# Kernel tuning notes

Hardware: AMD Instinct MI355X
Metric: run time of the kernel (lower is better)

The kernel has to match this reference:

```python
import jax, jax.numpy as jnp
import numpy as np

B = 8192          # batch of scenes
H = 20            # human_num
O = 10            # other_robot_num
IN = 13           # input_dim
SELF = 6          # self_state_dim
AG = IN - SELF    # agent_state_dim = 7
E1, E2 = 256, 128 # wr_dims / wh_dims
HID = 32          # hardcoded hidden_channels in Graphgnn
FIN = 128         # final_state_dim
P1, P2, P3 = 256, 128, 1  # planning_dims
NE = 8            # number of hetero edge types
# edge-type index convention:
# 0 robot->human, 1 human->robot, 2 other->robot, 3 robot->other,
# 4 other->human, 5 human->other, 6 human->human, 7 other->other


def setup_inputs() -> dict:
    key = jax.random.key(0)
    ks = iter(jax.random.split(key, 40))
    def nrm(shape, scale=0.05):
        return jax.random.normal(next(ks), shape, jnp.float32) * scale
    inp = {}
    inp["state"] = jax.random.normal(next(ks), (B, H + O, IN), jnp.float32)
    inp["dropout"] = 0  # unused by forward (kept for signature fidelity)
    # w_r: SELF -> E1 -> E2 (last_relu=True)
    inp["wr_W0"] = nrm((SELF, E1)); inp["wr_b0"] = nrm((E1,))
    inp["wr_W1"] = nrm((E1, E2));   inp["wr_b1"] = nrm((E2,))
    # w_h: AG -> E1 -> E2
    inp["wh_W0"] = nrm((AG, E1));   inp["wh_b0"] = nrm((E1,))
    inp["wh_W1"] = nrm((E1, E2));   inp["wh_b1"] = nrm((E2,))
    # w_o: AG -> E1 -> E2
    inp["wo_W0"] = nrm((AG, E1));   inp["wo_b0"] = nrm((E1,))
    inp["wo_W1"] = nrm((E1, E2));   inp["wo_b1"] = nrm((E2,))
    # per-edge-type GraphConv params (PyG GraphConv: lin_rel has bias, lin_root has none)
    inp["c1_relW"]  = nrm((NE, E2, HID)); inp["c1_relb"]  = nrm((NE, HID))
    inp["c1_rootW"] = nrm((NE, E2, HID))
    inp["c2_relW"]  = nrm((NE, HID, FIN)); inp["c2_relb"]  = nrm((NE, FIN))
    inp["c2_rootW"] = nrm((NE, HID, FIN))
    # value_net: FIN -> P1 -> P2 -> P3 (no final relu)
    inp["v_W0"] = nrm((FIN, P1)); inp["v_b0"] = nrm((P1,))
    inp["v_W1"] = nrm((P1, P2));  inp["v_b1"] = nrm((P2,))
    inp["v_W2"] = nrm((P2, P3));  inp["v_b2"] = nrm((P3,))
    return inp


def _mlp2(x, W0, b0, W1, b1, last_relu):
    h = jax.nn.relu(x @ W0 + b0)
    h = h @ W1 + b1
    return jax.nn.relu(h) if last_relu else h


def _hetero_conv(xr, xh, xo, relW, relb, rootW):
    # xr: [B,1,D], xh: [B,H,D], xo: [B,O,D]
    # GraphConv per edge type: out_dst = lin_root(x_dst) + lin_rel(sum of src messages)
    # graph is complete bipartite (sence) / complete-minus-self (affect),
    # so aggregations are closed-form sums.
    lin  = lambda x, i: jnp.einsum('bnd,do->bno', x, relW[i]) + relb[i]
    root = lambda x, i: jnp.einsum('bnd,do->bno', x, rootW[i])
    sh = xh.sum(axis=1, keepdims=True)  # [B,1,D] sum over humans
    so = xo.sum(axis=1, keepdims=True)  # [B,1,D] sum over other robots
    # robot receives: human->robot (1), other->robot (2)
    out_r = lin(sh, 1) + root(xr, 1) + lin(so, 2) + root(xr, 2)
    # human receives: robot->human (0), other->human (4), human->human (6)
    out_h = (lin(xr, 0) + root(xh, 0)
             + lin(so, 4) + root(xh, 4)
             + lin(sh - xh, 6) + root(xh, 6))
    # other receives: robot->other (3), human->other (5), other->other (7)
    out_o = (lin(xr, 3) + root(xo, 3)
             + lin(sh, 5) + root(xo, 5)
             + lin(so - xo, 7) + root(xo, 7))
    return out_r, out_h, out_o


def reference(state, dropout,
              wr_W0, wr_b0, wr_W1, wr_b1,
              wh_W0, wh_b0, wh_W1, wh_b1,
              wo_W0, wo_b0, wo_W1, wo_b1,
              c1_relW, c1_relb, c1_rootW,
              c2_relW, c2_relb, c2_rootW,
              v_W0, v_b0, v_W1, v_b1, v_W2, v_b2):
    self_state = state[:, 0, :SELF]          # [B, SELF]
    human_states = state[:, :H, SELF:]       # [B, H, AG]
    other_states = state[:, H:, SELF:]       # [B, O, AG]
    er = _mlp2(self_state, wr_W0, wr_b0, wr_W1, wr_b1, True)[:, None, :]  # [B,1,E2]
    eh = _mlp2(human_states, wh_W0, wh_b0, wh_W1, wh_b1, True)            # [B,H,E2]
    eo = _mlp2(other_states, wo_W0, wo_b0, wo_W1, wo_b1, True)            # [B,O,E2]
    r, h, o = _hetero_conv(er, eh, eo, c1_relW, c1_relb, c1_rootW)
    r, h, o = jax.nn.relu(r), jax.nn.relu(h), jax.nn.relu(o)
    r, h, o = _hetero_conv(r, h, o, c2_relW, c2_relb, c2_rootW)
    r = jax.nn.relu(r)
    hr = r[:, 0, :]                           # robot node per scene, [B, FIN]
    v = jax.nn.relu(hr @ v_W0 + v_b0)
    v = jax.nn.relu(v @ v_W1 + v_b1)
    v = v @ v_W2 + v_b2                       # [B, 1]
    return v
```

## Files before the change

### kernel.cpp

```cpp
#include <hip/hip_runtime.h>
#include <hip/hip_bf16.h>
#include <stdint.h>

#define BATCH 8192
#define NSTATE 30
#define DIN 13
#define E1 256
#define E2 128

typedef short bf16x8 __attribute__((ext_vector_type(8)));
typedef float f32x4 __attribute__((ext_vector_type(4)));
typedef __bf16 bf16x2_t __attribute__((ext_vector_type(2)));

__device__ __forceinline__ unsigned short f2b(float f) {
    return __builtin_bit_cast(unsigned short, (__bf16)f);
}
__device__ __forceinline__ float b2f(unsigned short b) {
    return __uint_as_float((unsigned)b << 16);
}
__device__ __forceinline__ unsigned pack2(float a, float b) {
    bf16x2_t v = {(__bf16)fmaxf(a, 0.f), (__bf16)fmaxf(b, 0.f)};
    return __builtin_bit_cast(unsigned, v);
}
__device__ __forceinline__ unsigned pack2n(float a, float b) {
    bf16x2_t v = {(__bf16)a, (__bf16)b};
    return __builtin_bit_cast(unsigned, v);
}

__device__ __forceinline__ f32x4 pin_f4(f32x4 v) {
    uint4 u = __builtin_bit_cast(uint4, v);
    asm volatile("" : "+v"(u.x), "+v"(u.y), "+v"(u.z), "+v"(u.w));
    return __builtin_bit_cast(f32x4, u);
}

__device__ __forceinline__ float wcat_val(int k, int m, const float* relW, const float* rootW) {
    int part = k >> 7, c = k & 127, grp = m >> 5, mm = m & 31;
    int off = c * 32 + mm;
    if (part == 0) return (grp == 0) ? rootW[4096 + off] + rootW[8192 + off]
                        : (grp == 1) ? relW[off] : relW[3*4096 + off];
    if (part == 1) return (grp == 0) ? relW[1*4096 + off]
                        : (grp == 1) ? relW[6*4096 + off] : relW[5*4096 + off];
    return (grp == 0) ? relW[2*4096 + off]
         : (grp == 1) ? relW[4*4096 + off] : relW[7*4096 + off];
}
__device__ __forceinline__ float wc2_val(int k, int n, const float* relW, const float* rootW) {
    int grp = k >> 5, kk = k & 31;
    int off = kk * 128 + n;
    if (grp == 0) return rootW[4096 + off] + rootW[8192 + off];
    if (grp == 1) return relW[4096 + off];
    return relW[8192 + off];
}

__global__ void k_prep(const float* __restrict__ c1_relW, const float* __restrict__ c1_relb,
                       const float* __restrict__ c1_rootW,
                       const float* __restrict__ c2_relW, const float* __restrict__ c2_relb,
                       const float* __restrict__ c2_rootW,
                       const float* __restrict__ wh_W0, const float* __restrict__ wh_W1,
                       const float* __restrict__ wo_W0, const float* __restrict__ wo_W1,
                       const float* __restrict__ wr_W0, const float* __restrict__ wr_W1,
                       const float* __restrict__ v_W0, const float* __restrict__ v_W1,
                       const float* __restrict__ b0h, const float* __restrict__ b0o,
                       const float* __restrict__ b0r,
                       float* __restrict__ bcat, float* __restrict__ bc2,
                       unsigned short* __restrict__ W0b_h, unsigned short* __restrict__ W0b_o,
                       unsigned short* __restrict__ W0b_r,
                       unsigned short* __restrict__ W1f_h, unsigned short* __restrict__ W1f_o,
                       unsigned short* __restrict__ W1f_r,
                       unsigned short* __restrict__ Mf_h, unsigned short* __restrict__ Mf_o,
                       unsigned short* __restrict__ Wcatf, unsigned short* __restrict__ Wc2f,
                       unsigned short* __restrict__ vW0f, unsigned short* __restrict__ vW1f)
{
    int gid = blockIdx.x * blockDim.x + threadIdx.x;
    int gsz = gridDim.x * blockDim.x;

    for (int i = gid; i < 96; i += gsz) {
        int grp = i >> 5, mm = i & 31;
        float v;
        if (grp == 0)      v = c1_relb[32 + mm] + c1_relb[64 + mm];
        else if (grp == 1) v = c1_relb[mm] + c1_relb[128 + mm] + c1_relb[192 + mm];
        else               v = c1_relb[96 + mm] + c1_relb[160 + mm] + c1_relb[224 + mm];
        bcat[i] = v;
    }
    for (int i = gid; i < 128; i += gsz) bc2[i] = c2_relb[128 + i] + c2_relb[256 + i];

    for (int i = gid; i < 2048; i += gsz) {
        int n = i >> 3, j = i & 7;
        W0b_h[i] = (j < 7) ? f2b(wh_W0[j * 256 + n]) : f2b(b0h[n]);
        W0b_o[i] = (j < 7) ? f2b(wo_W0[j * 256 + n]) : f2b(b0o[n]);
        W0b_r[i] = (j < 6) ? f2b(wr_W0[j * 256 + n])
                 : (j == 6) ? f2b(b0r[n]) : (unsigned short)0;
    }
    for (int i = gid; i < 32768; i += gsz) {
        int j = i & 7, l = (i >> 3) & 63, nt = (i >> 9) & 7, ks = i >> 12;
        int kk = ((j >> 2) * 8 + ks) * 16 + (l >> 4) * 4 + (j & 3);
        int n = nt * 16 + (l & 15);
        W1f_h[i] = f2b(wh_W1[kk * 128 + n]);
        W1f_o[i] = f2b(wo_W1[kk * 128 + n]);
        W1f_r[i] = f2b(wr_W1[kk * 128 + n]);
    }
    for (int i = gid; i < 4096; i += gsz) {
        int j = i & 7, l = (i >> 3) & 63, nt = (i >> 9) & 1, ks = i >> 10;
        int kk = ((j >> 2) * 4 + ks) * 16 + (l >> 4) * 4 + (j & 3);
        int n = nt * 16 + (l & 15);
        int i0 = kk * 32 + n;
        Mf_h[i] = f2b(c1_rootW[i0] + c1_rootW[4*4096 + i0] + c1_rootW[6*4096 + i0] - c1_relW[6*4096 + i0]);
        Mf_o[i] = f2b(c1_rootW[3*4096 + i0] + c1_rootW[5*4096 + i0] + c1_rootW[7*4096 + i0] - c1_relW[7*4096 + i0]);
    }
    for (int i = gid; i < 36864; i += gsz) {
        int j = i & 7, l = (i >> 3) & 63, rem = i >> 9;
        int nt = rem % 6, ks = rem / 6;
        int k = ks * 32 + (l >> 4) * 8 + j;
        int n = nt * 16 + (l & 15);
        Wcatf[i] = f2b(wcat_val(k, n, c1_relW, c1_rootW));
    }
    for (int i = gid; i < 12288; i += gsz) {
        int j = i & 7, l = (i >> 3) & 63, rem = i >> 9;
        int nt = rem & 7, ks = rem >> 3;
        int k = ks * 32 + (l >> 4) * 8 + j;
        int n = nt * 16 + (l & 15);
        Wc2f[i] = f2b(wc2_val(k, n, c2_relW, c2_rootW));
    }
    for (int i = gid; i < 32768; i += gsz) {
        int j = i & 7, l = (i >> 3) & 63, rem = i >> 9;
        int nt = rem & 15, ks = rem >> 4;
        int k = ks * 32 + (l >> 4) * 8 + j;
        int n = nt * 16 + (l & 15);
        vW0f[i] = f2b(v_W0[k * 256 + n]);
    }
    for (int i = gid; i < 32768; i += gsz) {
        int j = i & 7, l = (i >> 3) & 63, rem = i >> 9;
        int nt = rem & 7, ks = rem >> 3;
        int k = ks * 32 + (l >> 4) * 8 + j;
        int n = nt * 16 + (l & 15);
        vW1f[i] = f2b(v_W1[k * 128 + n]);
    }
}

#define SM_W0   0
#define SM_MF   4096
#define SM_W1   12288
#define SM_B1   77824
#define SM_HS   78336
#define SM_SZ   (78336 + 16 * 16 * 136 * 2)

template<int NPB, int NODE0, int INOFF, int INDIM, bool TAIL>
__device__ __forceinline__ void mlp_blockE(
    int blkrow0, const float* __restrict__ state,
    const unsigned short* __restrict__ W0b_g,
    const unsigned short* __restrict__ W1f_g, const float* __restrict__ b1,
    const unsigned short* __restrict__ Mf_g,
    unsigned short* __restrict__ tR, float* __restrict__ sumB,
    unsigned short* __restrict__ eR, char* smem)
{
    unsigned short* W0s = (unsigned short*)(smem + SM_W0);
    unsigned short* Mfs = (unsigned short*)(smem + SM_MF);
    unsigned short* W1s = (unsigned short*)(smem + SM_W1);
    float* b1s          = (float*)(smem + SM_B1);

    const int t = threadIdx.x;
    const int lane = t & 63;
    const int w = t >> 6;
    const int l15 = lane & 15;
    const int quad = lane >> 4;
    const int R0 = blkrow0 + w * 64;
    unsigned short* ew = (unsigned short*)(smem + SM_HS) + w * (16 * 136);

    if (t < 256) ((uint4*)W0s)[t] = ((const uint4*)W0b_g)[t];
    if (t >= 256 && t < 384) b1s[t - 256] = b1[t - 256];
    #pragma unroll
    for (int i = 0; i < 4; ++i)
        ((uint4*)W1s)[t + 1024 * i] = ((const uint4*)W1f_g)[t + 1024 * i];
    if constexpr (TAIL) {
        if (t >= 512 && t < 1024) ((uint4*)Mfs)[t - 512] = ((const uint4*)Mf_g)[t - 512];
    }
    __syncthreads();

    f32x4 bias1[8];
    #pragma unroll
    for (int nt = 0; nt < 8; ++nt) {
        float4 bb = *(const float4*)(b1s + nt * 16 + quad * 4);
        bias1[nt] = pin_f4((f32x4){bb.x, bb.y, bb.z, bb.w});
    }

    float s0 = 0.f, s1 = 0.f;
    int bcur = R0 / NPB;

    float xf[INDIM];
    #pragma unroll 1
    for (int dummy = 0; dummy < 1; ++dummy) {
        if (quad == 0) {
            int grow = R0 + l15;
            int b = grow / NPB;
            int n = grow - b * NPB + NODE0;
            const float* xp = state + ((size_t)b * NSTATE + n) * DIN + INOFF;
            #pragma unroll
            for (int j = 0; j < INDIM; ++j) xf[j] = xp[j];
        }
    }

    for (int sub = 0; sub < 4; ++sub) {
        const int wrow0 = R0 + sub * 16;

        bf16x8 bx = {};
        if (quad == 0) {
            #pragma unroll
            for (int j = 0; j < INDIM; ++j)
                bx[j] = (short)f2b(xf[j]);
            bx[INDIM] = (short)0x3F80;
        }
        if (sub < 3 && quad == 0) {
            int grow = wrow0 + 16 + l15;
            int b = grow / NPB;
            int n = grow - b * NPB + NODE0;
            const float* xp = state + ((size_t)b * NSTATE + n) * DIN + INOFF;
            #pragma unroll
            for (int j = 0; j < INDIM; ++j) xf[j] = xp[j];
        }

        f32x4 a1[16];
        #pragma unroll
        for (int nt = 0; nt < 16; ++nt) {
            bf16x8 aw = {};
            if (quad == 0)
                aw = *(const bf16x8*)(W0s + (nt * 16 + l15) * 8);
            f32x4 c = {0.f, 0.f, 0.f, 0.f};
            a1[nt] = __builtin_amdgcn_mfma_f32_16x16x32_bf16(aw, bx, c, 0, 0, 0);
        }

        bf16x8 bh[8];
        #pragma unroll
        for (int ks = 0; ks < 8; ++ks) {
            uint4 u;
            u.x = pack2(a1[ks][0], a1[ks][1]);
            u.y = pack2(a1[ks][2], a1[ks][3]);
            u.z = pack2(a1[ks + 8][0], a1[ks + 8][1]);
            u.w = pack2(a1[ks + 8][2], a1[ks + 8][3]);
            bh[ks] = __builtin_bit_cast(bf16x8, u);
        }

        f32x4 acc[8];
        #pragma unroll
        for (int nt = 0; nt < 8; ++nt) acc[nt] = bias1[nt];
        #pragma unroll
        for (int ks = 0; ks < 8; ++ks) {
            #pragma unroll
            for (int nt = 0; nt < 8; ++nt) {
                bf16x8 aw = *(const bf16x8*)(W1s + ((ks * 8 + nt) * 64 + lane) * 8);
                acc[nt] = __builtin_amdgcn_mfma_f32_16x16x32_bf16(aw, bh[ks], acc[nt], 0, 0, 0);
            }
        }

        uint2 pv[8];
        #pragma unroll
        for (int nt = 0; nt < 8; ++nt)
            pv[nt] = (uint2){pack2(acc[nt][0], acc[nt][1]), pack2(acc[nt][2], acc[nt][3])};

        if constexpr (TAIL) {
            __asm__ __volatile__("s_waitcnt lgkmcnt(0)" ::: "memory");
            #pragma unroll
            for (int nt = 0; nt < 8; ++nt)
                *(uint2*)(ew + l15 * 136 + nt * 16 + quad * 4) = pv[nt];

            f32x4 tacc[2] = {{0.f,0.f,0.f,0.f},{0.f,0.f,0.f,0.f}};
            #pragma unroll
            for (int ks = 0; ks < 4; ++ks) {
                uint4 ua;
                ua.x = pv[ks].x; ua.y = pv[ks].y;
                ua.z = pv[ks + 4].x; ua.w = pv[ks + 4].y;
                bf16x8 ae = __builtin_bit_cast(bf16x8, ua);
                #pragma unroll
                for (int nt = 0; nt < 2; ++nt) {
                    bf16x8 bm = *(const bf16x8*)(Mfs + ((ks * 2 + nt) * 64 + lane) * 8);
                    tacc[nt] = __builtin_amdgcn_mfma_f32_16x16x32_bf16(bm, ae, tacc[nt], 0, 0, 0);
                }
            }
            #pragma unroll
            for (int nt = 0; nt < 2; ++nt) {
                uint2 tv = {pack2n(tacc[nt][0], tacc[nt][1]), pack2n(tacc[nt][2], tacc[nt][3])};
                *(uint2*)(tR + (size_t)(wrow0 + l15) * 32 + nt * 16 + quad * 4) = tv;
            }

            #pragma unroll
            for (int r = 0; r < 16; ++r) {
                int b = (wrow0 + r) / NPB;
                if (b != bcur) {
                    bool interior = (bcur * NPB >= R0) && ((bcur + 1) * NPB <= R0 + 64);
                    float* dst = sumB + (size_t)bcur * 128 + 2 * lane;
                    if (interior) { dst[0] = s0; dst[1] = s1; }
                    else { atomicAdd(dst, s0); atomicAdd(dst + 1, s1); }
                    s0 = 0.f; s1 = 0.f; bcur = b;
                }
                unsigned v = *(const unsigned*)(ew + r * 136 + lane * 2);
                s0 += b2f((unsigned short)v);
                s1 += b2f((unsigned short)(v >> 16));
            }
            if (sub == 3) {
                bool interior = (bcur * NPB >= R0) && ((bcur + 1) * NPB <= R0 + 64);
                float* dst = sumB + (size_t)bcur * 128 + 2 * lane;
                if (interior) { dst[0] = s0; dst[1] = s1; }
                else { atomicAdd(dst, s0); atomicAdd(dst + 1, s1); }
            }
        } else {
            #pragma unroll
            for (int nt = 0; nt < 8; ++nt)
                *(uint2*)(eR + (size_t)(wrow0 + l15) * 128 + nt * 16 + quad * 4) = pv[nt];
        }
        __asm__ __volatile__("" ::: "memory");
    }
}

__global__ __launch_bounds__(1024, 1) void k_mlpE(
    const float* __restrict__ state,
    const unsigned short* __restrict__ W0b_h,
    const unsigned short* __restrict__ W1f_h, const float* __restrict__ b1_h,
    const unsigned short* __restrict__ Mf_h, unsigned short* __restrict__ tR_h,
    float* __restrict__ shB,
    const unsigned short* __restrict__ W0b_o,
    const unsigned short* __restrict__ W1f_o, const float* __restrict__ b1_o,
    const unsigned short* __restrict__ Mf_o, unsigned short* __restrict__ tR_o,
    float* __restrict__ soB,
    const unsigned short* __restrict__ W0b_r,
    const unsigned short* __restrict__ W1f_r, const float* __restrict__ b1_r,
    unsigned short* __restrict__ eR)
{
    __shared__ __align__(16) char smem[SM_SZ];
    int bid = blockIdx.x;
    if (bid < 160)
        mlp_blockE<20, 0, 6, 7, true>(bid * 1024, state, W0b_h, W1f_h, b1_h,
                                      Mf_h, tR_h, shB, nullptr, smem);
    else if (bid < 240)
        mlp_blockE<10, 20, 6, 7, true>((bid - 160) * 1024, state, W0b_o, W1f_o, b1_o,
                                       Mf_o, tR_o, soB, nullptr, smem);
    else
        mlp_blockE<1, 0, 0, 6, false>((bid - 240) * 1024, state, W0b_r, W1f_r, b1_r,
                                      nullptr, nullptr, nullptr, eR, smem);
}

__global__ __launch_bounds__(256, 2) void k_tail(
    const unsigned short* __restrict__ eR,
    const float* __restrict__ shB, const float* __restrict__ soB,
    const unsigned short* __restrict__ tR_h, const unsigned short* __restrict__ tR_o,
    const unsigned short* __restrict__ Wcatf, const float* __restrict__ bcat,
    const unsigned short* __restrict__ Wc2f, const float* __restrict__ bc2,
    const unsigned short* __restrict__ vW0f, const float* __restrict__ vb0,
    const unsigned short* __restrict__ vW1f, const float* __restrict__ vb1,
    const float* __restrict__ vW2, const float* __restrict__ vb2,
    float* __restrict__ out)
{
    __shared__ __align__(16) char sm[33024];
    unsigned short* Ub  = (unsigned short*)(sm);
    unsigned short* V1b = (unsigned short*)(sm);
    unsigned short* Vb  = (unsigned short*)(sm + 12800);
    float* chL          = (float*)(sm + 16128);
    float* coL          = (float*)(sm + 18176);
    unsigned short* Hb  = (unsigned short*)(sm + 20224);
    float* V2b          = (float*)(sm + 24576);

    const int t = threadIdx.x, lane = t & 63, w = t >> 6;
    const int l15 = lane & 15, quad = lane >> 4;
    const int b0 = blockIdx.x * 16;
    const int rowb = quad * 4;

    {
        int b = t >> 4, q = t & 15;
        ((uint4*)(Ub + b * 400))[q] = ((const uint4*)(eR + (size_t)(b0 + b) * 128))[q];
    }
    for (int idx = t; idx < 4096; idx += 256) {
        int b = idx >> 8, kk = idx & 255;
        float v = (kk < 128) ? shB[(size_t)(b0 + b) * 128 + kk]
                             : soB[(size_t)(b0 + b) * 128 + kk - 128];
        Ub[b * 400 + 128 + kk] = f2b(v);
    }
    __syncthreads();

    for (int nt = w; nt < 6; nt += 4) {
        float bias = bcat[nt * 16 + l15];
        f32x4 acc = {bias, bias, bias, bias};
        #pragma unroll
        for (int ks = 0; ks < 12; ++ks) {
            bf16x8 a = *(const bf16x8*)(Ub + l15 * 400 + ks * 32 + quad * 8);
            bf16x8 bw = *(const bf16x8*)(Wcatf + ((ks * 6 + nt) * 64 + lane) * 8);
            acc = __builtin_amdgcn_mfma_f32_16x16x32_bf16(a, bw, acc, 0, 0, 0);
        }
        int n = nt * 16 + l15;
        #pragma unroll
        for (int reg = 0; reg < 4; ++reg) {
            float v = acc[reg];
            int b = rowb + reg;
            if (n < 32)      Vb[b * 104 + n] = f2b(fmaxf(v, 0.f));
            else if (n < 64) chL[b * 32 + (n - 32)] = v;
            else             coL[b * 32 + (n - 64)] = v;
        }
    }
    __syncthreads();

    for (int idx = t; idx < 512; idx += 256) {
        int b = idx >> 5, m = idx & 31;
        float ch = chL[b * 32 + m];
        const unsigned short* p = tR_h + (size_t)(b0 + b) * 20 * 32 + m;
        float s = 0.f;
        #pragma unroll
        for (int n = 0; n < 20; ++n) s += fmaxf(ch + b2f(p[n * 32]), 0.f);
        Vb[b * 104 + 32 + m] = f2b(s);
        float co = coL[b * 32 + m];
        const unsigned short* p2 = tR_o + (size_t)(b0 + b) * 10 * 32 + m;
        float s2 = 0.f;
        #pragma unroll
        for (int n = 0; n < 10; ++n) s2 += fmaxf(co + b2f(p2[n * 32]), 0.f);
        Vb[b * 104 + 64 + m] = f2b(s2);
    }
    __syncthreads();

    {
        f32x4 acc[2];
        #pragma unroll
        for (int q = 0; q < 2; ++q) {
            int nt = w + q * 4;
            float bias = bc2[nt * 16 + l15];
            acc[q] = (f32x4){bias, bias, bias, bias};
        }
        #pragma unroll
        for (int ks = 0; ks < 3; ++ks) {
            bf16x8 a = *(const bf16x8*)(Vb + l15 * 104 + ks * 32 + quad * 8);
            #pragma unroll
            for (int q = 0; q < 2; ++q) {
                int nt = w + q * 4;
                bf16x8 bw = *(const bf16x8*)(Wc2f + ((ks * 8 + nt) * 64 + lane) * 8);
                acc[q] = __builtin_amdgcn_mfma_f32_16x16x32_bf16(a, bw, acc[q], 0, 0, 0);
            }
        }
        #pragma unroll
        for (int q = 0; q < 2; ++q) {
            int nt = w + q * 4;
            #pragma unroll
            for (int reg = 0; reg < 4; ++reg)
                Hb[(rowb + reg) * 136 + nt * 16 + l15] = f2b(fmaxf(acc[q][reg], 0.f));
        }
    }
    __syncthreads();

    {
        f32x4 acc[4];
        #pragma unroll
        for (int q = 0; q < 4; ++q) {
            int nt = w + q * 4;
            float bias = vb0[nt * 16 + l15];
            acc[q] = (f32x4){bias, bias, bias, bias};
        }
        #pragma unroll
        for (int ks = 0; ks < 4; ++ks) {
            bf16x8 a = *(const bf16x8*)(Hb + l15 * 136 + ks * 32 + quad * 8);
            #pragma unroll
            for (int q = 0; q < 4; ++q) {
                int nt = w + q * 4;
                bf16x8 bw = *(const bf16x8*)(vW0f + ((ks * 16 + nt) * 64 + lane) * 8);
                acc[q] = __builtin_amdgcn_mfma_f32_16x16x32_bf16(a, bw, acc[q], 0, 0, 0);
            }
        }
        __syncthreads();
        #pragma unroll
        for (int q = 0; q < 4; ++q) {
            int nt = w + q * 4;
            #pragma unroll
            for (int reg = 0; reg < 4; ++reg)
                V1b[(rowb + reg) * 264 + nt * 16 + l15] = f2b(fmaxf(acc[q][reg], 0.f));
        }
    }
    __syncthreads();

    {
        f32x4 acc[2];
        #pragma unroll
        for (int q = 0; q < 2; ++q) {
            int nt = w + q * 4;
            float bias = vb1[nt * 16 + l15];
            acc[q] = (f32x4){bias, bias, bias, bias};
        }
        #pragma unroll
        for (int ks = 0; ks < 8; ++ks) {
            bf16x8 a = *(const bf16x8*)(V1b + l15 * 264 + ks * 32 + quad * 8);
            #pragma unroll
            for (int q = 0; q < 2; ++q) {
                int nt = w + q * 4;
                bf16x8 bw = *(const bf16x8*)(vW1f + ((ks * 8 + nt) * 64 + lane) * 8);
                acc[q] = __builtin_amdgcn_mfma_f32_16x16x32_bf16(a, bw, acc[q], 0, 0, 0);
            }
        }
        #pragma unroll
        for (int q = 0; q < 2; ++q) {
            int nt = w + q * 4;
            #pragma unroll
            for (int reg = 0; reg < 4; ++reg)
                V2b[(rowb + reg) * 132 + nt * 16 + l15] = fmaxf(acc[q][reg], 0.f);
        }
    }
    __syncthreads();

    if (t < 128) {
        int b = t >> 3, j = t & 7;
        float v = 0.f;
        #pragma unroll
        for (int k = 0; k < 16; ++k)
            v = fmaf(V2b[b * 132 + j * 16 + k], vW2[j * 16 + k], v);
        v += __shfl_down(v, 4, 8);
        v += __shfl_down(v, 2, 8);
        v += __shfl_down(v, 1, 8);
        if (j == 0) out[b0 + b] = v + vb2[0];
    }
}

extern "C" void kernel_launch(void* const* d_in, const int* in_sizes, int n_in,
                              void* d_out, int out_size, void* d_ws, size_t ws_size,
                              hipStream_t stream)
{
    const float* state   = (const float*)d_in[0];
    const float* wr_W0   = (const float*)d_in[2];
    const float* wr_b0   = (const float*)d_in[3];
    const float* wr_W1   = (const float*)d_in[4];
    const float* wr_b1   = (const float*)d_in[5];
    const float* wh_W0   = (const float*)d_in[6];
    const float* wh_b0   = (const float*)d_in[7];
    const float* wh_W1   = (const float*)d_in[8];
    const float* wh_b1   = (const float*)d_in[9];
    const float* wo_W0   = (const float*)d_in[10];
    const float* wo_b0   = (const float*)d_in[11];
    const float* wo_W1   = (const float*)d_in[12];
    const float* wo_b1   = (const float*)d_in[13];
    const float* c1_relW = (const float*)d_in[14];
    const float* c1_relb = (const float*)d_in[15];
    const float* c1_rootW= (const float*)d_in[16];
    const float* c2_relW = (const float*)d_in[17];
    const float* c2_relb = (const float*)d_in[18];
    const float* c2_rootW= (const float*)d_in[19];
    const float* v_W0    = (const float*)d_in[20];
    const float* v_b0    = (const float*)d_in[21];
    const float* v_W1    = (const float*)d_in[22];
    const float* v_b1    = (const float*)d_in[23];
    const float* v_W2    = (const float*)d_in[24];
    const float* v_b2    = (const float*)d_in[25];

    char* ws = (char*)d_ws;
    size_t off = 0;
    auto alloc = [&](size_t bytes) -> char* {
        char* p = ws + off;
        off = (off + bytes + 255) & ~(size_t)255;
        return p;
    };
    float* shB  = (float*)alloc((size_t)BATCH * 128 * 4);
    float* soB  = (float*)alloc((size_t)BATCH * 128 * 4);
    unsigned short* tR_h = (unsigned short*)alloc((size_t)163840 * 32 * 2);
    unsigned short* tR_o = (unsigned short*)alloc((size_t)81920 * 32 * 2);
    unsigned short* eR   = (unsigned short*)alloc((size_t)BATCH * 128 * 2);
    float* bcat = (float*)alloc(96 * 4);
    float* bc2  = (float*)alloc(128 * 4);
    unsigned short* W0b_h = (unsigned short*)alloc(2048 * 2);
    unsigned short* W0b_o = (unsigned short*)alloc(2048 * 2);
    unsigned short* W0b_r = (unsigned short*)alloc(2048 * 2);
    unsigned short* W1f_h = (unsigned short*)alloc(32768 * 2);
    unsigned short* W1f_o = (unsigned short*)alloc(32768 * 2);
    unsigned short* W1f_r = (unsigned short*)alloc(32768 * 2);
    unsigned short* Mf_h  = (unsigned short*)alloc(4096 * 2);
    unsigned short* Mf_o  = (unsigned short*)alloc(4096 * 2);
    unsigned short* Wcatf = (unsigned short*)alloc(36864 * 2);
    unsigned short* Wc2f  = (unsigned short*)alloc(12288 * 2);
    unsigned short* vW0f  = (unsigned short*)alloc(32768 * 2);
    unsigned short* vW1f  = (unsigned short*)alloc(32768 * 2);
    (void)ws_size; (void)in_sizes; (void)n_in; (void)out_size;

    hipMemsetAsync(shB, 0, (size_t)2 * BATCH * 128 * 4, stream);

    k_prep<<<256, 256, 0, stream>>>(c1_relW, c1_relb, c1_rootW, c2_relW, c2_relb, c2_rootW,
                                    wh_W0, wh_W1, wo_W0, wo_W1, wr_W0, wr_W1, v_W0, v_W1,
                                    wh_b0, wo_b0, wr_b0,
                                    bcat, bc2, W0b_h, W0b_o, W0b_r, W1f_h, W1f_o, W1f_r,
                                    Mf_h, Mf_o, Wcatf, Wc2f, vW0f, vW1f);

    k_mlpE<<<248, 1024, 0, stream>>>(state,
                                     W0b_h, W1f_h, wh_b1, Mf_h, tR_h, shB,
                                     W0b_o, W1f_o, wo_b1, Mf_o, tR_o, soB,
                                     W0b_r, W1f_r, wr_b1, eR);

    k_tail<<<512, 256, 0, stream>>>(eR, shB, soB, tR_h, tR_o,
                                    Wcatf, bcat, Wc2f, bc2, vW0f, v_b0, vW1f, v_b1,
                                    v_W2, v_b2, (float*)d_out);
}
```

Measured before the change: 157.5 us.

## Switch encoder MLP to 32x32x16 MFMA tiles with bias folded into GEMM

Rewrites the per-node encoder MLP in k_mlpE to use 32x32x16 bf16 MFMA instead of 16x16x32. Each wave now handles two 32-row subtiles instead of four 16-row subtiles, and the first-layer output is fed straight into the second layer per 32-column chunk. The second-layer bias is folded in as an extra K-step that multiplies by a ones vector, replacing the preloaded bias registers. k_prep re-lays out W0, W1 and M to match the new fragment layout. This targets the weight-load and instruction overhead of small MFMA tiles, but raises register pressure (f32x16 accumulators) and adds an extra MFMA step for the bias.

```diff
diff --git a/kernel.cpp b/kernel.cpp
--- a/kernel.cpp
+++ b/kernel.cpp
@@ -10,6 +10,7 @@
 
 typedef short bf16x8 __attribute__((ext_vector_type(8)));
 typedef float f32x4 __attribute__((ext_vector_type(4)));
+typedef float f32x16 __attribute__((ext_vector_type(16)));
 typedef __bf16 bf16x2_t __attribute__((ext_vector_type(2)));
 
 __device__ __forceinline__ unsigned short f2b(float f) {
@@ -25,12 +26,6 @@
 __device__ __forceinline__ unsigned pack2n(float a, float b) {
     bf16x2_t v = {(__bf16)a, (__bf16)b};
     return __builtin_bit_cast(unsigned, v);
-}
-
-__device__ __forceinline__ f32x4 pin_f4(f32x4 v) {
-    uint4 u = __builtin_bit_cast(uint4, v);
-    asm volatile("" : "+v"(u.x), "+v"(u.y), "+v"(u.z), "+v"(u.w));
-    return __builtin_bit_cast(f32x4, u);
 }
 
 __device__ __forceinline__ float wcat_val(int k, int m, const float* relW, const float* rootW) {
@@ -61,6 +56,8 @@
                        const float* __restrict__ v_W0, const float* __restrict__ v_W1,
                        const float* __restrict__ b0h, const float* __restrict__ b0o,
                        const float* __restrict__ b0r,
+                       const float* __restrict__ b1h, const float* __restrict__ b1o,
+                       const float* __restrict__ b1r,
                        float* __restrict__ bcat, float* __restrict__ bc2,
                        unsigned short* __restrict__ W0b_h, unsigned short* __restrict__ W0b_o,
                        unsigned short* __restrict__ W0b_r,
@@ -83,26 +80,44 @@
     }
     for (int i = gid; i < 128; i += gsz) bc2[i] = c2_relb[128 + i] + c2_relb[256 + i];
 
-    for (int i = gid; i < 2048; i += gsz) {
-        int n = i >> 3, j = i & 7;
-        W0b_h[i] = (j < 7) ? f2b(wh_W0[j * 256 + n]) : f2b(b0h[n]);
-        W0b_o[i] = (j < 7) ? f2b(wo_W0[j * 256 + n]) : f2b(b0o[n]);
-        W0b_r[i] = (j < 6) ? f2b(wr_W0[j * 256 + n])
-                 : (j == 6) ? f2b(b0r[n]) : (unsigned short)0;
-    }
-    for (int i = gid; i < 32768; i += gsz) {
-        int j = i & 7, l = (i >> 3) & 63, nt = (i >> 9) & 7, ks = i >> 12;
-        int kk = ((j >> 2) * 8 + ks) * 16 + (l >> 4) * 4 + (j & 3);
-        int n = nt * 16 + (l & 15);
-        W1f_h[i] = f2b(wh_W1[kk * 128 + n]);
-        W1f_o[i] = f2b(wo_W1[kk * 128 + n]);
-        W1f_r[i] = f2b(wr_W1[kk * 128 + n]);
-    }
     for (int i = gid; i < 4096; i += gsz) {
-        int j = i & 7, l = (i >> 3) & 63, nt = (i >> 9) & 1, ks = i >> 10;
-        int kk = ((j >> 2) * 4 + ks) * 16 + (l >> 4) * 4 + (j & 3);
-        int n = nt * 16 + (l & 15);
-        int i0 = kk * 32 + n;
+        int j = i & 7, l = (i >> 3) & 63, nh = i >> 9;
+        int col = nh * 32 + (l & 31);
+        unsigned short vh = 0, vo = 0, vr = 0;
+        if (l < 32) {
+            vh = (j < 7) ? f2b(wh_W0[j * 256 + col]) : f2b(b0h[col]);
+            vo = (j < 7) ? f2b(wo_W0[j * 256 + col]) : f2b(b0o[col]);
+            vr = (j < 6) ? f2b(wr_W0[j * 256 + col])
+               : (j == 6) ? f2b(b0r[col]) : (unsigned short)0;
+        }
+        W0b_h[i] = vh; W0b_o[i] = vo; W0b_r[i] = vr;
+    }
+    for (int i = gid; i < 34816; i += gsz) {
+        int j = i & 7, l = (i >> 3) & 63, rem = i >> 9;
+        int nt = rem & 3, ks = rem >> 2;
+        int ecol = nt * 32 + (l & 31);
+        int hh = l >> 5;
+        unsigned short vh, vo, vr;
+        if (ks < 16) {
+            int r = (ks & 1) * 8 + j;
+            int hcol = (ks >> 1) * 32 + (r & 3) + 8 * (r >> 2) + 4 * hh;
+            vh = f2b(wh_W1[hcol * 128 + ecol]);
+            vo = f2b(wo_W1[hcol * 128 + ecol]);
+            vr = f2b(wr_W1[hcol * 128 + ecol]);
+        } else {
+            bool on = (l < 32) && (j == 0);
+            vh = on ? f2b(b1h[ecol]) : (unsigned short)0;
+            vo = on ? f2b(b1o[ecol]) : (unsigned short)0;
+            vr = on ? f2b(b1r[ecol]) : (unsigned short)0;
+        }
+        W1f_h[i] = vh; W1f_o[i] = vo; W1f_r[i] = vr;
+    }
+    for (int i = gid; i < 4096; i += gsz) {
+        int j = i & 7, l = (i >> 3) & 63, kt = i >> 9;
+        int hh = l >> 5, s = kt & 1, r = s * 8 + j;
+        int ecol = (kt >> 1) * 32 + (r & 3) + 8 * (r >> 2) + 4 * hh;
+        int tcol = l & 31;
+        int i0 = ecol * 32 + tcol;
         Mf_h[i] = f2b(c1_rootW[i0] + c1_rootW[4*4096 + i0] + c1_rootW[6*4096 + i0] - c1_relW[6*4096 + i0]);
         Mf_o[i] = f2b(c1_rootW[3*4096 + i0] + c1_rootW[5*4096 + i0] + c1_rootW[7*4096 + i0] - c1_relW[7*4096 + i0]);
     }
@@ -137,17 +152,16 @@
 }
 
 #define SM_W0   0
-#define SM_MF   4096
-#define SM_W1   12288
-#define SM_B1   77824
-#define SM_HS   78336
-#define SM_SZ   (78336 + 16 * 16 * 136 * 2)
+#define SM_MF   8192
+#define SM_W1   16384
+#define SM_HS   86016
+#define SM_SZ   (86016 + 16 * 16 * 136 * 2)
 
 template<int NPB, int NODE0, int INOFF, int INDIM, bool TAIL>
 __device__ __forceinline__ void mlp_blockE(
     int blkrow0, const float* __restrict__ state,
     const unsigned short* __restrict__ W0b_g,
-    const unsigned short* __restrict__ W1f_g, const float* __restrict__ b1,
+    const unsigned short* __restrict__ W1f_g,
     const unsigned short* __restrict__ Mf_g,
     unsigned short* __restrict__ tR, float* __restrict__ sumB,
     unsigned short* __restrict__ eR, char* smem)
@@ -155,155 +169,160 @@
     unsigned short* W0s = (unsigned short*)(smem + SM_W0);
     unsigned short* Mfs = (unsigned short*)(smem + SM_MF);
     unsigned short* W1s = (unsigned short*)(smem + SM_W1);
-    float* b1s          = (float*)(smem + SM_B1);
 
     const int t = threadIdx.x;
     const int lane = t & 63;
     const int w = t >> 6;
-    const int l15 = lane & 15;
-    const int quad = lane >> 4;
+    const int l31 = lane & 31;
+    const int hi = lane >> 5;
     const int R0 = blkrow0 + w * 64;
     unsigned short* ew = (unsigned short*)(smem + SM_HS) + w * (16 * 136);
 
-    if (t < 256) ((uint4*)W0s)[t] = ((const uint4*)W0b_g)[t];
-    if (t >= 256 && t < 384) b1s[t - 256] = b1[t - 256];
+    if (t < 512) ((uint4*)W0s)[t] = ((const uint4*)W0b_g)[t];
+    if constexpr (TAIL) {
+        if (t >= 512) ((uint4*)Mfs)[t - 512] = ((const uint4*)Mf_g)[t - 512];
+    }
     #pragma unroll
     for (int i = 0; i < 4; ++i)
         ((uint4*)W1s)[t + 1024 * i] = ((const uint4*)W1f_g)[t + 1024 * i];
-    if constexpr (TAIL) {
-        if (t >= 512 && t < 1024) ((uint4*)Mfs)[t - 512] = ((const uint4*)Mf_g)[t - 512];
-    }
+    if (t < 256) ((uint4*)W1s)[4096 + t] = ((const uint4*)W1f_g)[4096 + t];
     __syncthreads();
 
-    f32x4 bias1[8];
-    #pragma unroll
-    for (int nt = 0; nt < 8; ++nt) {
-        float4 bb = *(const float4*)(b1s + nt * 16 + quad * 4);
-        bias1[nt] = pin_f4((f32x4){bb.x, bb.y, bb.z, bb.w});
-    }
+    bf16x8 bones = {};
+    if (lane < 32) bones[0] = (short)0x3F80;
 
     float s0 = 0.f, s1 = 0.f;
     int bcur = R0 / NPB;
 
     float xf[INDIM];
-    #pragma unroll 1
-    for (int dummy = 0; dummy < 1; ++dummy) {
-        if (quad == 0) {
-            int grow = R0 + l15;
+    if (lane < 32) {
+        int grow = R0 + l31;
+        int b = grow / NPB;
+        int n = grow - b * NPB + NODE0;
+        const float* xp = state + ((size_t)b * NSTATE + n) * DIN + INOFF;
+        #pragma unroll
+        for (int j = 0; j < INDIM; ++j) xf[j] = xp[j];
+    }
+
+    for (int sub = 0; sub < 2; ++sub) {
+        const int wrow0 = R0 + sub * 32;
+
+        bf16x8 bx = {};
+        if (lane < 32) {
+            #pragma unroll
+            for (int j = 0; j < INDIM; ++j) bx[j] = (short)f2b(xf[j]);
+            bx[INDIM] = (short)0x3F80;
+        }
+        if (sub < 1 && lane < 32) {
+            int grow = wrow0 + 32 + l31;
             int b = grow / NPB;
             int n = grow - b * NPB + NODE0;
             const float* xp = state + ((size_t)b * NSTATE + n) * DIN + INOFF;
             #pragma unroll
             for (int j = 0; j < INDIM; ++j) xf[j] = xp[j];
         }
-    }
-
-    for (int sub = 0; sub < 4; ++sub) {
-        const int wrow0 = R0 + sub * 16;
-
-        bf16x8 bx = {};
-        if (quad == 0) {
-            #pragma unroll
-            for (int j = 0; j < INDIM; ++j)
-                bx[j] = (short)f2b(xf[j]);
-            bx[INDIM] = (short)0x3F80;
-        }
-        if (sub < 3 && quad == 0) {
-            int grow = wrow0 + 16 + l15;
-            int b = grow / NPB;
-            int n = grow - b * NPB + NODE0;
-            const float* xp = state + ((size_t)b * NSTATE + n) * DIN + INOFF;
-            #pragma unroll
-            for (int j = 0; j < INDIM; ++j) xf[j] = xp[j];
-        }
-
-        f32x4 a1[16];
-        #pragma unroll
-        for (int nt = 0; nt < 16; ++nt) {
-            bf16x8 aw = {};
-            if (quad == 0)
-                aw = *(const bf16x8*)(W0s + (nt * 16 + l15) * 8);
-            f32x4 c = {0.f, 0.f, 0.f, 0.f};
-            a1[nt] = __builtin_amdgcn_mfma_f32_16x16x32_bf16(aw, bx, c, 0, 0, 0);
-        }
-
-        bf16x8 bh[8];
-        #pragma unroll
-        for (int ks = 0; ks < 8; ++ks) {
-            uint4 u;
-            u.x = pack2(a1[ks][0], a1[ks][1]);
-            u.y = pack2(a1[ks][2], a1[ks][3]);
-            u.z = pack2(a1[ks + 8][0], a1[ks + 8][1]);
-            u.w = pack2(a1[ks + 8][2], a1[ks + 8][3]);
-            bh[ks] = __builtin_bit_cast(bf16x8, u);
-        }
-
-        f32x4 acc[8];
-        #pragma unroll
-        for (int nt = 0; nt < 8; ++nt) acc[nt] = bias1[nt];
-        #pragma unroll
-        for (int ks = 0; ks < 8; ++ks) {
-            #pragma unroll
-            for (int nt = 0; nt < 8; ++nt) {
-                bf16x8 aw = *(const bf16x8*)(W1s + ((ks * 8 + nt) * 64 + lane) * 8);
-                acc[nt] = __builtin_amdgcn_mfma_f32_16x16x32_bf16(aw, bh[ks], acc[nt], 0, 0, 0);
-            }
-        }
-
-        uint2 pv[8];
-        #pragma unroll
-        for (int nt = 0; nt < 8; ++nt)
-            pv[nt] = (uint2){pack2(acc[nt][0], acc[nt][1]), pack2(acc[nt][2], acc[nt][3])};
+
+        f32x16 acc[4];
+        #pragma unroll
+        for (int nt = 0; nt < 4; ++nt) { f32x16 z = {}; acc[nt] = z; }
+        #pragma unroll
+        for (int nh = 0; nh < 8; ++nh) {
+            bf16x8 aw0 = *(const bf16x8*)(W0s + (nh * 64 + lane) * 8);
+            f32x16 z = {};
+            f32x16 a1 = __builtin_amdgcn_mfma_f32_32x32x16_bf16(aw0, bx, z, 0, 0, 0);
+            uint4 ua, ub;
+            ua.x = pack2(a1[0], a1[1]);   ua.y = pack2(a1[2], a1[3]);
+            ua.z = pack2(a1[4], a1[5]);   ua.w = pack2(a1[6], a1[7]);
+            ub.x = pack2(a1[8], a1[9]);   ub.y = pack2(a1[10], a1[11]);
+            ub.z = pack2(a1[12], a1[13]); ub.w = pack2(a1[14], a1[15]);
+            bf16x8 bhA = __builtin_bit_cast(bf16x8, ua);
+            bf16x8 bhB = __builtin_bit_cast(bf16x8, ub);
+            #pragma unroll
+            for (int nt = 0; nt < 4; ++nt) {
+                bf16x8 aw = *(const bf16x8*)(W1s + (((2 * nh) * 4 + nt) * 64 + lane) * 8);
+                acc[nt] = __builtin_amdgcn_mfma_f32_32x32x16_bf16(aw, bhA, acc[nt], 0, 0, 0);
+            }
+            #pragma unroll
+            for (int nt = 0; nt < 4; ++nt) {
+                bf16x8 aw = *(const bf16x8*)(W1s + (((2 * nh + 1) * 4 + nt) * 64 + lane) * 8);
+                acc[nt] = __builtin_amdgcn_mfma_f32_32x32x16_bf16(aw, bhB, acc[nt], 0, 0, 0);
+            }
+        }
+        #pragma unroll
+        for (int nt = 0; nt < 4; ++nt) {
+            bf16x8 aw = *(const bf16x8*)(W1s + ((64 + nt) * 64 + lane) * 8);
+            acc[nt] = __builtin_amdgcn_mfma_f32_32x32x16_bf16(aw, bones, acc[nt], 0, 0, 0);
+        }
+
+        unsigned pvu[4][8];
+        #pragma unroll
+        for (int nt = 0; nt < 4; ++nt)
+            #pragma unroll
+            for (int p = 0; p < 8; ++p)
+                pvu[nt][p] = pack2(acc[nt][2 * p], acc[nt][2 * p + 1]);
 
         if constexpr (TAIL) {
-            __asm__ __volatile__("s_waitcnt lgkmcnt(0)" ::: "memory");
-            #pragma unroll
-            for (int nt = 0; nt < 8; ++nt)
-                *(uint2*)(ew + l15 * 136 + nt * 16 + quad * 4) = pv[nt];
-
-            f32x4 tacc[2] = {{0.f,0.f,0.f,0.f},{0.f,0.f,0.f,0.f}};
-            #pragma unroll
-            for (int ks = 0; ks < 4; ++ks) {
-                uint4 ua;
-                ua.x = pv[ks].x; ua.y = pv[ks].y;
-                ua.z = pv[ks + 4].x; ua.w = pv[ks + 4].y;
+            f32x16 tacc = {};
+            #pragma unroll
+            for (int kt = 0; kt < 8; ++kt) {
+                const int nt = kt >> 1, s = kt & 1;
+                uint4 ua = {pvu[nt][4 * s], pvu[nt][4 * s + 1],
+                            pvu[nt][4 * s + 2], pvu[nt][4 * s + 3]};
                 bf16x8 ae = __builtin_bit_cast(bf16x8, ua);
+                bf16x8 bm = *(const bf16x8*)(Mfs + (kt * 64 + lane) * 8);
+                tacc = __builtin_amdgcn_mfma_f32_32x32x16_bf16(bm, ae, tacc, 0, 0, 0);
+            }
+            {
+                unsigned short* tRrow = tR + (size_t)(wrow0 + l31) * 32 + 4 * hi;
                 #pragma unroll
-                for (int nt = 0; nt < 2; ++nt) {
-                    bf16x8 bm = *(const bf16x8*)(Mfs + ((ks * 2 + nt) * 64 + lane) * 8);
-                    tacc[nt] = __builtin_amdgcn_mfma_f32_16x16x32_bf16(bm, ae, tacc[nt], 0, 0, 0);
+                for (int q = 0; q < 4; ++q) {
+                    uint2 tv = {pack2n(tacc[4 * q], tacc[4 * q + 1]),
+                                pack2n(tacc[4 * q + 2], tacc[4 * q + 3])};
+                    *(uint2*)(tRrow + 8 * q) = tv;
                 }
             }
             #pragma unroll
-            for (int nt = 0; nt < 2; ++nt) {
-                uint2 tv = {pack2n(tacc[nt][0], tacc[nt][1]), pack2n(tacc[nt][2], tacc[nt][3])};
-                *(uint2*)(tR + (size_t)(wrow0 + l15) * 32 + nt * 16 + quad * 4) = tv;
-            }
-
-            #pragma unroll
-            for (int r = 0; r < 16; ++r) {
-                int b = (wrow0 + r) / NPB;
-                if (b != bcur) {
-                    bool interior = (bcur * NPB >= R0) && ((bcur + 1) * NPB <= R0 + 64);
-                    float* dst = sumB + (size_t)bcur * 128 + 2 * lane;
-                    if (interior) { dst[0] = s0; dst[1] = s1; }
-                    else { atomicAdd(dst, s0); atomicAdd(dst + 1, s1); }
-                    s0 = 0.f; s1 = 0.f; bcur = b;
+            for (int half = 0; half < 2; ++half) {
+                __asm__ __volatile__("s_waitcnt lgkmcnt(0)" ::: "memory");
+                if ((l31 >> 4) == half) {
+                    unsigned short* er = ew + (l31 & 15) * 136 + 4 * hi;
+                    #pragma unroll
+                    for (int nt = 0; nt < 4; ++nt)
+                        #pragma unroll
+                        for (int q = 0; q < 4; ++q)
+                            *(uint2*)(er + nt * 32 + 8 * q) =
+                                (uint2){pvu[nt][2 * q], pvu[nt][2 * q + 1]};
                 }
-                unsigned v = *(const unsigned*)(ew + r * 136 + lane * 2);
-                s0 += b2f((unsigned short)v);
-                s1 += b2f((unsigned short)(v >> 16));
-            }
-            if (sub == 3) {
+                const int grow0 = wrow0 + half * 16;
+                #pragma unroll
+                for (int r = 0; r < 16; ++r) {
+                    int b = (grow0 + r) / NPB;
+                    if (b != bcur) {
+                        bool interior = (bcur * NPB >= R0) && ((bcur + 1) * NPB <= R0 + 64);
+                        float* dst = sumB + (size_t)bcur * 128 + 2 * lane;
+                        if (interior) { dst[0] = s0; dst[1] = s1; }
+                        else { atomicAdd(dst, s0); atomicAdd(dst + 1, s1); }
+                        s0 = 0.f; s1 = 0.f; bcur = b;
+                    }
+                    unsigned v = *(const unsigned*)(ew + r * 136 + lane * 2);
+                    s0 += b2f((unsigned short)v);
+                    s1 += b2f((unsigned short)(v >> 16));
+                }
+            }
+            if (sub == 1) {
                 bool interior = (bcur * NPB >= R0) && ((bcur + 1) * NPB <= R0 + 64);
                 float* dst = sumB + (size_t)bcur * 128 + 2 * lane;
                 if (interior) { dst[0] = s0; dst[1] = s1; }
                 else { atomicAdd(dst, s0); atomicAdd(dst + 1, s1); }
             }
         } else {
-            #pragma unroll
-            for (int nt = 0; nt < 8; ++nt)
-                *(uint2*)(eR + (size_t)(wrow0 + l15) * 128 + nt * 16 + quad * 4) = pv[nt];
+            unsigned short* eRrow = eR + (size_t)(wrow0 + l31) * 128 + 4 * hi;
+            #pragma unroll
+            for (int nt = 0; nt < 4; ++nt)
+                #pragma unroll
+                for (int q = 0; q < 4; ++q)
+                    *(uint2*)(eRrow + nt * 32 + 8 * q) =
+                        (uint2){pvu[nt][2 * q], pvu[nt][2 * q + 1]};
         }
         __asm__ __volatile__("" ::: "memory");
     }
@@ -312,27 +331,27 @@
 __global__ __launch_bounds__(1024, 1) void k_mlpE(
     const float* __restrict__ state,
     const unsigned short* __restrict__ W0b_h,
-    const unsigned short* __restrict__ W1f_h, const float* __restrict__ b1_h,
+    const unsigned short* __restrict__ W1f_h,
     const unsigned short* __restrict__ Mf_h, unsigned short* __restrict__ tR_h,
     float* __restrict__ shB,
     const unsigned short* __restrict__ W0b_o,
-    const unsigned short* __restrict__ W1f_o, const float* __restrict__ b1_o,
+    const unsigned short* __restrict__ W1f_o,
     const unsigned short* __restrict__ Mf_o, unsigned short* __restrict__ tR_o,
     float* __restrict__ soB,
     const unsigned short* __restrict__ W0b_r,
-    const unsigned short* __restrict__ W1f_r, const float* __restrict__ b1_r,
+    const unsigned short* __restrict__ W1f_r,
     unsigned short* __restrict__ eR)
 {
     __shared__ __align__(16) char smem[SM_SZ];
     int bid = blockIdx.x;
     if (bid < 160)
-        mlp_blockE<20, 0, 6, 7, true>(bid * 1024, state, W0b_h, W1f_h, b1_h,
+        mlp_blockE<20, 0, 6, 7, true>(bid * 1024, state, W0b_h, W1f_h,
                                       Mf_h, tR_h, shB, nullptr, smem);
     else if (bid < 240)
-        mlp_blockE<10, 20, 6, 7, true>((bid - 160) * 1024, state, W0b_o, W1f_o, b1_o,
+        mlp_blockE<10, 20, 6, 7, true>((bid - 160) * 1024, state, W0b_o, W1f_o,
                                        Mf_o, tR_o, soB, nullptr, smem);
     else
-        mlp_blockE<1, 0, 0, 6, false>((bid - 240) * 1024, state, W0b_r, W1f_r, b1_r,
+        mlp_blockE<1, 0, 0, 6, false>((bid - 240) * 1024, state, W0b_r, W1f_r,
                                       nullptr, nullptr, nullptr, eR, smem);
 }
 
@@ -553,12 +572,12 @@
     unsigned short* eR   = (unsigned short*)alloc((size_t)BATCH * 128 * 2);
     float* bcat = (float*)alloc(96 * 4);
     float* bc2  = (float*)alloc(128 * 4);
-    unsigned short* W0b_h = (unsigned short*)alloc(2048 * 2);
-    unsigned short* W0b_o = (unsigned short*)alloc(2048 * 2);
-    unsigned short* W0b_r = (unsigned short*)alloc(2048 * 2);
-    unsigned short* W1f_h = (unsigned short*)alloc(32768 * 2);
-    unsigned short* W1f_o = (unsigned short*)alloc(32768 * 2);
-    unsigned short* W1f_r = (unsigned short*)alloc(32768 * 2);
+    unsigned short* W0b_h = (unsigned short*)alloc(4096 * 2);
+    unsigned short* W0b_o = (unsigned short*)alloc(4096 * 2);
+    unsigned short* W0b_r = (unsigned short*)alloc(4096 * 2);
+    unsigned short* W1f_h = (unsigned short*)alloc(34816 * 2);
+    unsigned short* W1f_o = (unsigned short*)alloc(34816 * 2);
+    unsigned short* W1f_r = (unsigned short*)alloc(34816 * 2);
     unsigned short* Mf_h  = (unsigned short*)alloc(4096 * 2);
     unsigned short* Mf_o  = (unsigned short*)alloc(4096 * 2);
     unsigned short* Wcatf = (unsigned short*)alloc(36864 * 2);
@@ -571,14 +590,14 @@
 
     k_prep<<<256, 256, 0, stream>>>(c1_relW, c1_relb, c1_rootW, c2_relW, c2_relb, c2_rootW,
                                     wh_W0, wh_W1, wo_W0, wo_W1, wr_W0, wr_W1, v_W0, v_W1,
-                                    wh_b0, wo_b0, wr_b0,
+                                    wh_b0, wo_b0, wr_b0, wh_b1, wo_b1, wr_b1,
                                     bcat, bc2, W0b_h, W0b_o, W0b_r, W1f_h, W1f_o, W1f_r,
                                     Mf_h, Mf_o, Wcatf, Wc2f, vW0f, vW1f);
 
     k_mlpE<<<248, 1024, 0, stream>>>(state,
-                                     W0b_h, W1f_h, wh_b1, Mf_h, tR_h, shB,
-                                     W0b_o, W1f_o, wo_b1, Mf_o, tR_o, soB,
-                                     W0b_r, W1f_r, wr_b1, eR);
+                                     W0b_h, W1f_h, Mf_h, tR_h, shB,
+                                     W0b_o, W1f_o, Mf_o, tR_o, soB,
+                                     W0b_r, W1f_r, eR);
 
     k_tail<<<512, 256, 0, stream>>>(eR, shB, soB, tR_h, tR_o,
                                     Wcatf, bcat, Wc2f, bc2, vW0f, v_b0, vW1f, v_b1,
```

Measured after the change: 153.6 us, median of 2. 1.03x faster.
